# Kernel optimization log

Hardware: AMD Instinct MI355X
Metric: run time of the kernel (lower is better)

## Reference

```python
import jax, jax.numpy as jnp
import numpy as np

EPS = 1e-5

def knn_gather(x, k):
    # x: [B,N,C] -> neighbors [B,N,k,C] (k nearest incl. self, DGCNN style)
    sq = jnp.sum(x * x, axis=-1)                                   # [B,N]
    dist = sq[:, :, None] + sq[:, None, :] - 2.0 * jnp.einsum('bnc,bmc->bnm', x, x)
    _, idx = jax.lax.top_k(-dist, k)                               # [B,N,k]
    neigh = jax.vmap(lambda xb, ib: xb[ib])(x, idx)                # [B,N,k,C]
    return neigh

def local_cov(neigh):
    # neigh: [B,N,k,C] -> flattened per-point covariance [B,N,C*C]
    k = neigh.shape[2]
    c = neigh - jnp.mean(neigh, axis=2, keepdims=True)
    cov = jnp.einsum('bnkc,bnkd->bncd', c, c) / k
    return cov.reshape(cov.shape[0], cov.shape[1], -1)

def bn(x, g, b):
    # BatchNorm1d training-mode forward on [B,N,C]: stats over (B,N), biased var
    m = jnp.mean(x, axis=(0, 1))
    v = jnp.var(x, axis=(0, 1))
    return (x - m) * jax.lax.rsqrt(v + EPS) * g + b

def setup_inputs() -> dict:
    key = jax.random.key(0)
    ks = jax.random.split(key, 8)
    B, N = 2, 8192
    d = {}
    d['x'] = jax.random.normal(ks[0], (B, N, 3), dtype=jnp.float32)
    # conv weights stored as [in, out] (1x1 Conv1d == per-point matmul)
    def w(k_, i, o):
        return jax.random.normal(k_, (i, o), dtype=jnp.float32) * (1.0 / np.sqrt(i))
    d['W1'] = w(ks[1], 12, 64);   d['g1'] = jnp.ones(64);   d['b1'] = jnp.zeros(64)
    d['W2'] = w(ks[2], 64, 64);   d['g2'] = jnp.ones(64);   d['b2'] = jnp.zeros(64)
    d['W3'] = w(ks[3], 64, 64);   d['g3'] = jnp.ones(64);   d['b3'] = jnp.zeros(64)
    d['gW1'] = w(ks[4], 64, 128);  d['gg1'] = jnp.ones(128);  d['gb1'] = jnp.zeros(128)
    d['gW2'] = w(ks[5], 128, 1024); d['gg2'] = jnp.ones(1024); d['gb2'] = jnp.zeros(1024)
    d['W4'] = w(ks[6], 1024, 512); d['g4'] = jnp.ones(512);  d['b4'] = jnp.zeros(512)
    return d

def reference(x, W1, g1, b1, W2, g2, b2, W3, g3, b3,
              gW1, gg1, gb1, gW2, gg2, gb2, W4, g4, b4):
    # GBEncoder forward
    neigh = knn_gather(x, 32)                                   # [B,N,32,3]
    h = jnp.concatenate([x, local_cov(neigh)], axis=-1)         # [B,N,12]
    h = jax.nn.relu(bn(h @ W1, g1, b1))                         # [B,N,64]
    h = jax.nn.relu(bn(h @ W2, g2, b2))
    h = jax.nn.relu(bn(h @ W3, g3, b3))
    # GraphLayer 1: knn(k=8) gather -> max over neighbors -> 1x1 conv + BN + LeakyReLU
    n = jnp.max(knn_gather(h, 8), axis=2)                       # [B,N,64]
    h = jax.nn.leaky_relu(bn(n @ gW1, gg1, gb1), 0.01)          # [B,N,128]
    # GraphLayer 2
    n = jnp.max(knn_gather(h, 8), axis=2)                       # [B,N,128]
    h = jax.nn.leaky_relu(bn(n @ gW2, gg2, gb2), 0.01)          # [B,N,1024]
    # global max-pool over points, keepdim -> [B,1,1024]
    h = jnp.max(h, axis=1, keepdims=True)
    return jax.nn.relu(bn(h @ W4, g4, b4))                      # [B,1,512]
```

## Files before the change

### kernel.cpp

```cpp
#include <hip/hip_runtime.h>
#include <cfloat>
#include <cstdint>

#define NPTS 8192
#define NBROWS 16384

typedef unsigned long long u64;
typedef unsigned short ushortT;
typedef __attribute__((ext_vector_type(8))) short short8;
typedef __attribute__((ext_vector_type(4))) float f32x4;

__device__ __forceinline__ unsigned fkey(float f) {
  unsigned u = __float_as_uint(f);
  return (u & 0x80000000u) ? ~u : (u | 0x80000000u);
}
__device__ __forceinline__ float fdecode(unsigned k) {
  unsigned u = (k & 0x80000000u) ? (k ^ 0x80000000u) : ~k;
  return __uint_as_float(u);
}
__device__ __forceinline__ float bf2f(ushortT v) {
  return __uint_as_float(((unsigned)v) << 16);
}
__device__ __forceinline__ unsigned rne16(float x, float& hf) {
  unsigned u = __float_as_uint(x);
  unsigned r = (u + 0x7FFFu + ((u >> 16) & 1u)) >> 16;
  hf = __uint_as_float(r << 16);
  return r;
}

template <int K>
__device__ __forceinline__ void chain_insert(u64 (&kk)[K], u64 key) {
  #pragma unroll
  for (int q = K - 1; q >= 1; --q) {
    bool cm1 = key < kk[q - 1];
    bool cq  = key < kk[q];
    kk[q] = cm1 ? kk[q - 1] : (cq ? key : kk[q]);
  }
  kk[0] = (key < kk[0]) ? key : kk[0];
}

__global__ __launch_bounds__(256) void sqx_kernel(const float* __restrict__ x,
                                                  float* __restrict__ sq) {
  int r = blockIdx.x * 256 + threadIdx.x;
  const float* xp = x + (size_t)r * 3;
  sq[r] = fmaf(xp[2], xp[2], fmaf(xp[1], xp[1], xp[0] * xp[0]));
}

__global__ __launch_bounds__(512, 4) void knn32_cov_kernel(const float* __restrict__ x,
                                                           const float* __restrict__ sqx,
                                                           float* __restrict__ feat) {
  __shared__ __align__(16) unsigned char smem[78080];
  float4* stage4 = (float4*)smem;
  unsigned* keyArea = (unsigned*)smem;
  unsigned* Trow = (unsigned*)(smem + 67584);
  unsigned* cnt  = (unsigned*)(smem + 67712);
  u64* apb = (u64*)(smem + 67840);

  const int t = threadIdx.x;
  const int r = t & 31, sub = t >> 5;
  const int rowBase = blockIdx.x * 32;
  const int batchBase = rowBase & ~(NPTS - 1);
  const int gRow = rowBase + r;

  const float xi0 = x[(size_t)gRow * 3 + 0];
  const float xi1 = x[(size_t)gRow * 3 + 1];
  const float xi2 = x[(size_t)gRow * 3 + 2];
  const float sqi = sqx[gRow];

  unsigned K[32];
  #pragma unroll
  for (int q = 0; q < 32; ++q) K[q] = 0xFFFFFFFFu;

  for (int round = 0; round < 4; ++round) {
    __syncthreads();
    #pragma unroll
    for (int u = 0; u < 4; ++u) {
      int pp = t + 512 * u;
      int s = pp >> 7, jj = pp & 127;
      int j = s * 512 + round * 128 + jj;
      const float* xp = x + (size_t)(batchBase + j) * 3;
      float4 w;
      w.x = xp[0]; w.y = xp[1]; w.z = xp[2];
      w.w = sqx[batchBase + j];
      stage4[pp] = w;
    }
    __syncthreads();
    const float4* st = stage4 + sub * 128;
    for (int jj = 0; jj < 128; ++jj) {
      float4 w = st[jj];
      float dot = fmaf(xi2, w.z, fmaf(xi1, w.y, xi0 * w.x));
      float d = sqi + w.w - 2.0f * dot;
      unsigned key = fkey(d);
      #pragma unroll
      for (int q = 31; q >= 1; --q) K[q] = max(K[q - 1], min(key, K[q]));
      K[0] = min(key, K[0]);
    }
  }
  __syncthreads();
  {
    const int base = (sub * 32 + r) * 33;
    #pragma unroll
    for (int z = 0; z < 32; ++z) keyArea[base + z] = K[z];
  }
  __syncthreads();
  if (t < 32) {
    cnt[t] = 0u;
    unsigned P[16];
    #pragma unroll
    for (int s = 0; s < 16; ++s) P[s] = 0u;
    unsigned T = 0u;
    for (int step = 0; step < 32; ++step) {
      unsigned best = 0xFFFFFFFFu; int bs = 0;
      #pragma unroll
      for (int s = 0; s < 16; ++s) {
        unsigned v = keyArea[(s * 32 + t) * 33 + P[s]];
        if (v < best) { best = v; bs = s; }
      }
      T = best;
      #pragma unroll
      for (int s = 0; s < 16; ++s) P[s] += (s == bs);
    }
    Trow[t] = T;
  }
  __syncthreads();
  for (int round = 0; round < 4; ++round) {
    __syncthreads();
    #pragma unroll
    for (int u = 0; u < 4; ++u) {
      int pp = t + 512 * u;
      int s = pp >> 7, jj = pp & 127;
      int j = s * 512 + round * 128 + jj;
      const float* xp = x + (size_t)(batchBase + j) * 3;
      float4 w;
      w.x = xp[0]; w.y = xp[1]; w.z = xp[2];
      w.w = sqx[batchBase + j];
      stage4[pp] = w;
    }
    __syncthreads();
    const float4* st = stage4 + sub * 128;
    const unsigned T = Trow[r];
    for (int jj = 0; jj < 128; ++jj) {
      float4 w = st[jj];
      float dot = fmaf(xi2, w.z, fmaf(xi1, w.y, xi0 * w.x));
      float d = sqi + w.w - 2.0f * dot;
      unsigned key = fkey(d);
      if (key <= T) {
        int j = sub * 512 + round * 128 + jj;
        unsigned slot = atomicAdd(&cnt[r], 1u);
        if (slot < 40u) apb[r * 40 + slot] = ((u64)key << 16) | (unsigned)j;
      }
    }
  }
  __syncthreads();
  if (t < 32) {
    int n = (int)cnt[t]; if (n > 40) n = 40;
    u64 kk[32];
    #pragma unroll
    for (int q = 0; q < 32; ++q) kk[q] = ~0ULL;
    for (int i = 0; i < n; ++i) chain_insert<32>(kk, apb[t * 40 + i]);
    float sx = 0.f, sy = 0.f, sz = 0.f;
    #pragma unroll 4
    for (int z = 0; z < 32; ++z) {
      const float* xp = x + (size_t)(batchBase + (int)(kk[z] & 0xFFFFULL)) * 3;
      sx += xp[0]; sy += xp[1]; sz += xp[2];
    }
    const float m0 = sx * (1.f / 32.f), m1 = sy * (1.f / 32.f), m2 = sz * (1.f / 32.f);
    float c00 = 0, c01 = 0, c02 = 0, c11 = 0, c12 = 0, c22 = 0;
    #pragma unroll 4
    for (int z = 0; z < 32; ++z) {
      const float* xp = x + (size_t)(batchBase + (int)(kk[z] & 0xFFFFULL)) * 3;
      float a0 = xp[0] - m0, a1 = xp[1] - m1, a2 = xp[2] - m2;
      c00 = fmaf(a0, a0, c00); c01 = fmaf(a0, a1, c01); c02 = fmaf(a0, a2, c02);
      c11 = fmaf(a1, a1, c11); c12 = fmaf(a1, a2, c12); c22 = fmaf(a2, a2, c22);
    }
    const float inv = 1.f / 32.f;
    float* fp = feat + (size_t)(rowBase + t) * 12;
    fp[0] = xi0; fp[1] = xi1; fp[2] = xi2;
    fp[3] = c00 * inv; fp[4] = c01 * inv; fp[5] = c02 * inv;
    fp[6] = c01 * inv; fp[7] = c11 * inv; fp[8] = c12 * inv;
    fp[9] = c02 * inv; fp[10] = c12 * inv; fp[11] = c22 * inv;
  }
}

__global__ __launch_bounds__(64) void mm12_64_kernel(const float* __restrict__ feat,
                                                     const float* __restrict__ W,
                                                     float* __restrict__ y,
                                                     float* __restrict__ psum,
                                                     float* __restrict__ psq) {
  __shared__ __align__(16) float Ws[12 * 64];
  const int t = threadIdx.x;
  for (int u = t; u < 192; u += 64) ((float4*)Ws)[u] = ((const float4*)W)[u];
  __syncthreads();
  const int row = blockIdx.x * 64 + t;
  float in[12];
  {
    const float4* fp = (const float4*)(feat + (size_t)row * 12);
    float4 a = fp[0], b = fp[1], c = fp[2];
    in[0] = a.x; in[1] = a.y; in[2] = a.z; in[3] = a.w;
    in[4] = b.x; in[5] = b.y; in[6] = b.z; in[7] = b.w;
    in[8] = c.x; in[9] = c.y; in[10] = c.z; in[11] = c.w;
  }
  float acc[64];
  #pragma unroll
  for (int o = 0; o < 64; ++o) acc[o] = 0.f;
  #pragma unroll
  for (int i = 0; i < 12; ++i) {
    const float xi = in[i];
    #pragma unroll
    for (int og = 0; og < 16; ++og) {
      float4 w4 = *(const float4*)(Ws + i * 64 + og * 4);
      acc[og * 4 + 0] = fmaf(xi, w4.x, acc[og * 4 + 0]);
      acc[og * 4 + 1] = fmaf(xi, w4.y, acc[og * 4 + 1]);
      acc[og * 4 + 2] = fmaf(xi, w4.z, acc[og * 4 + 2]);
      acc[og * 4 + 3] = fmaf(xi, w4.w, acc[og * 4 + 3]);
    }
  }
  float4* yp = (float4*)(y + (size_t)row * 64);
  #pragma unroll
  for (int og = 0; og < 16; ++og)
    yp[og] = make_float4(acc[og * 4 + 0], acc[og * 4 + 1], acc[og * 4 + 2], acc[og * 4 + 3]);
  #pragma unroll 1
  for (int o = 0; o < 64; ++o) {
    float s = acc[o], q = acc[o] * acc[o];
    #pragma unroll
    for (int m = 1; m < 64; m <<= 1) { s += __shfl_xor(s, m); q += __shfl_xor(q, m); }
    if (t == 0) { psum[blockIdx.x * 64 + o] = s; psq[blockIdx.x * 64 + o] = q; }
  }
}

template <int OUT, bool BNRELU>
__global__ __launch_bounds__(64) void mm64_kernel(const float* __restrict__ src,
                                                  const float* __restrict__ W,
                                                  const float* __restrict__ scale,
                                                  const float* __restrict__ shift,
                                                  float* __restrict__ y,
                                                  float* __restrict__ psum,
                                                  float* __restrict__ psq) {
  __shared__ __align__(16) float Ws[64 * OUT];
  const int t = threadIdx.x;
  for (int u = t; u < 16 * OUT; u += 64) ((float4*)Ws)[u] = ((const float4*)W)[u];
  __syncthreads();
  const int row = blockIdx.x * 64 + t;
  float in[64];
  {
    const float4* sp = (const float4*)(src + (size_t)row * 64);
    #pragma unroll
    for (int u = 0; u < 16; ++u) {
      float4 v = sp[u];
      if (BNRELU) {
        v.x = fmaxf(fmaf(v.x, scale[u * 4 + 0], shift[u * 4 + 0]), 0.f);
        v.y = fmaxf(fmaf(v.y, scale[u * 4 + 1], shift[u * 4 + 1]), 0.f);
        v.z = fmaxf(fmaf(v.z, scale[u * 4 + 2], shift[u * 4 + 2]), 0.f);
        v.w = fmaxf(fmaf(v.w, scale[u * 4 + 3], shift[u * 4 + 3]), 0.f);
      }
      in[u * 4 + 0] = v.x; in[u * 4 + 1] = v.y; in[u * 4 + 2] = v.z; in[u * 4 + 3] = v.w;
    }
  }
  for (int half = 0; half < OUT / 64; ++half) {
    float acc[64];
    #pragma unroll
    for (int o = 0; o < 64; ++o) acc[o] = 0.f;
    #pragma unroll 4
    for (int i = 0; i < 64; ++i) {
      const float xi = in[i];
      #pragma unroll
      for (int og = 0; og < 16; ++og) {
        float4 w4 = *(const float4*)(Ws + i * OUT + half * 64 + og * 4);
        acc[og * 4 + 0] = fmaf(xi, w4.x, acc[og * 4 + 0]);
        acc[og * 4 + 1] = fmaf(xi, w4.y, acc[og * 4 + 1]);
        acc[og * 4 + 2] = fmaf(xi, w4.z, acc[og * 4 + 2]);
        acc[og * 4 + 3] = fmaf(xi, w4.w, acc[og * 4 + 3]);
      }
    }
    float4* yp = (float4*)(y + (size_t)row * OUT + half * 64);
    #pragma unroll
    for (int og = 0; og < 16; ++og)
      yp[og] = make_float4(acc[og * 4 + 0], acc[og * 4 + 1], acc[og * 4 + 2], acc[og * 4 + 3]);
    #pragma unroll 1
    for (int o = 0; o < 64; ++o) {
      float s = acc[o], q = acc[o] * acc[o];
      #pragma unroll
      for (int m = 1; m < 64; m <<= 1) { s += __shfl_xor(s, m); q += __shfl_xor(q, m); }
      if (t == 0) {
        psum[blockIdx.x * OUT + half * 64 + o] = s;
        psq[blockIdx.x * OUT + half * 64 + o] = q;
      }
    }
  }
}

template <int C>
__global__ void finP_kernel(const float* __restrict__ psum, const float* __restrict__ psq,
                            const float* __restrict__ g, const float* __restrict__ b,
                            float* __restrict__ scale, float* __restrict__ shift) {
  int c = threadIdx.x;
  float s = 0.f, q = 0.f;
  for (int bb = 0; bb < 256; ++bb) { s += psum[bb * C + c]; q += psq[bb * C + c]; }
  float m = s * (1.f / 16384.f);
  float v = q * (1.f / 16384.f) - m * m;
  float sc = g[c] * rsqrtf(v + 1e-5f);
  scale[c] = sc;
  shift[c] = b[c] - m * sc;
}

template <int C, bool LEAKY>
__global__ __launch_bounds__(256) void apply_kernel(const float* __restrict__ yraw,
                                                    const float* __restrict__ scale,
                                                    const float* __restrict__ shift,
                                                    ushortT* __restrict__ hbf,
                                                    float* __restrict__ sqout) {
  const int row = blockIdx.x * 256 + threadIdx.x;
  const float4* sp = (const float4*)(yraw + (size_t)row * C);
  ushortT* hb = hbf + (size_t)row * (3 * C);
  float sq = 0.f;
  #pragma unroll
  for (int g = 0; g < C / 8; ++g) {
    float e[8];
    #pragma unroll
    for (int half = 0; half < 2; ++half) {
      float4 v = sp[g * 2 + half];
      const int u = g * 2 + half;
      float4 o;
      o.x = fmaf(v.x, scale[u * 4 + 0], shift[u * 4 + 0]);
      o.y = fmaf(v.y, scale[u * 4 + 1], shift[u * 4 + 1]);
      o.z = fmaf(v.z, scale[u * 4 + 2], shift[u * 4 + 2]);
      o.w = fmaf(v.w, scale[u * 4 + 3], shift[u * 4 + 3]);
      if (LEAKY) {
        o.x = o.x > 0.f ? o.x : 0.01f * o.x;
        o.y = o.y > 0.f ? o.y : 0.01f * o.y;
        o.z = o.z > 0.f ? o.z : 0.01f * o.z;
        o.w = o.w > 0.f ? o.w : 0.01f * o.w;
      } else {
        o.x = fmaxf(o.x, 0.f); o.y = fmaxf(o.y, 0.f);
        o.z = fmaxf(o.z, 0.f); o.w = fmaxf(o.w, 0.f);
      }
      sq = fmaf(o.x, o.x, sq); sq = fmaf(o.y, o.y, sq);
      sq = fmaf(o.z, o.z, sq); sq = fmaf(o.w, o.w, sq);
      e[half * 4 + 0] = o.x; e[half * 4 + 1] = o.y;
      e[half * 4 + 2] = o.z; e[half * 4 + 3] = o.w;
    }
    unsigned pa[8], pb[8], pc[8];
    #pragma unroll
    for (int j = 0; j < 8; ++j) {
      float af, bf, cf;
      pa[j] = rne16(e[j], af);
      float r1 = e[j] - af;
      pb[j] = rne16(r1, bf);
      float r2 = r1 - bf;
      pc[j] = rne16(r2, cf);
    }
    uint4 va, vb, vc;
    va.x = pa[0] | (pa[1] << 16); va.y = pa[2] | (pa[3] << 16);
    va.z = pa[4] | (pa[5] << 16); va.w = pa[6] | (pa[7] << 16);
    vb.x = pb[0] | (pb[1] << 16); vb.y = pb[2] | (pb[3] << 16);
    vb.z = pb[4] | (pb[5] << 16); vb.w = pb[6] | (pb[7] << 16);
    vc.x = pc[0] | (pc[1] << 16); vc.y = pc[2] | (pc[3] << 16);
    vc.z = pc[4] | (pc[5] << 16); vc.w = pc[6] | (pc[7] << 16);
    *(uint4*)(hb + g * 8) = va;
    *(uint4*)(hb + C + g * 8) = vb;
    *(uint4*)(hb + 2 * C + g * 8) = vc;
  }
  sqout[row] = sq;
}

template <int C>
__global__ __launch_bounds__(256, 3) void knn8_kernel(const ushortT* __restrict__ hbf,
                                                      const float* __restrict__ sqh,
                                                      u64* __restrict__ plist) {
  static_assert(C == 64 || C == 128, "C");
  constexpr int STR = 3 * C + 8;
  constexpr int BSB = 64 * STR * 2;
  constexpr int SMB = BSB > 49152 ? BSB : 49152;
  __shared__ __align__(16) unsigned char smem[SMB];
  ushortT* Bs = (ushortT*)smem;
  u64* mb = (u64*)smem;
  __shared__ float sqB[64];

  const int t = threadIdx.x;
  const int l = t & 63, w = t >> 6;
  const int quad = l >> 4, fif = l & 15;
  const int rg = blockIdx.x >> 2, quarter = blockIdx.x & 3;
  const int rowBase = rg * 64;
  const int batchBase = rowBase & ~(NPTS - 1);

  constexpr int KS = C / 32;
  short8 aa[KS], ab[KS], ac[KS];
  {
    const int arow = rowBase + 16 * w + fif;
    const ushortT* ap = hbf + (size_t)arow * (3 * C);
    #pragma unroll
    for (int s = 0; s < KS; ++s) {
      aa[s] = *(const short8*)(ap + s * 32 + quad * 8);
      ab[s] = *(const short8*)(ap + C + s * 32 + quad * 8);
      ac[s] = *(const short8*)(ap + 2 * C + s * 32 + quad * 8);
    }
  }
  float sqA[4];
  #pragma unroll
  for (int r = 0; r < 4; ++r) sqA[r] = sqh[rowBase + 16 * w + quad * 4 + r];

  u64 L[4][8];
  #pragma unroll
  for (int r = 0; r < 4; ++r)
    #pragma unroll
    for (int z = 0; z < 8; ++z) L[r][z] = ~0ULL;

  constexpr int CPP = C / 8;
  constexpr int LOG = (CPP == 16) ? 4 : 3;

  for (int chunk = 0; chunk < 32; ++chunk) {
    const int cb = quarter * 2048 + chunk * 64;
    __syncthreads();
    {
      #pragma unroll
      for (int p = 0; p < 3; ++p) {
        #pragma unroll
        for (int z = 0; z < (64 * CPP) / 256; ++z) {
          int id = t + 256 * z;
          int col = id >> LOG, ch = id & (CPP - 1);
          uint4 v = *(const uint4*)(hbf + (size_t)(batchBase + cb + col) * (3 * C) + p * C + ch * 8);
          *(uint4*)(Bs + col * STR + p * C + ch * 8) = v;
        }
      }
      if (t < 64) sqB[t] = sqh[batchBase + cb + t];
    }
    __syncthreads();
    #pragma unroll
    for (int tile = 0; tile < 4; ++tile) {
      const int lcol = tile * 16 + fif;
      f32x4 acc0 = {0.f, 0.f, 0.f, 0.f};
      f32x4 acc1 = {0.f, 0.f, 0.f, 0.f};
      f32x4 acc2 = {0.f, 0.f, 0.f, 0.f};
      const ushortT* bp = Bs + lcol * STR + quad * 8;
      #pragma unroll
      for (int s = 0; s < KS; ++s) {
        short8 ba = *(const short8*)(bp + s * 32);
        short8 bb = *(const short8*)(bp + C + s * 32);
        short8 bc = *(const short8*)(bp + 2 * C + s * 32);
        acc0 = __builtin_amdgcn_mfma_f32_16x16x32_bf16(aa[s], ba, acc0, 0, 0, 0);
        acc1 = __builtin_amdgcn_mfma_f32_16x16x32_bf16(aa[s], bb, acc1, 0, 0, 0);
        acc2 = __builtin_amdgcn_mfma_f32_16x16x32_bf16(ab[s], ba, acc2, 0, 0, 0);
        acc0 = __builtin_amdgcn_mfma_f32_16x16x32_bf16(aa[s], bc, acc0, 0, 0, 0);
        acc1 = __builtin_amdgcn_mfma_f32_16x16x32_bf16(ac[s], ba, acc1, 0, 0, 0);
        acc2 = __builtin_amdgcn_mfma_f32_16x16x32_bf16(ab[s], bb, acc2, 0, 0, 0);
      }
      const float sb = sqB[lcol];
      const unsigned gcol = (unsigned)(cb + lcol);
      #pragma unroll
      for (int r = 0; r < 4; ++r) {
        float dot = acc0[r] + acc1[r] + acc2[r];
        float d = sqA[r] + sb - 2.0f * dot;
        u64 key = ((u64)fkey(d) << 16) | gcol;
        chain_insert<8>(L[r], key);
      }
    }
  }
  for (int rh = 0; rh < 2; ++rh) {
    __syncthreads();
    if ((w >> 1) == rh) {
      #pragma unroll
      for (int r = 0; r < 4; ++r) {
        int lr = (16 * w + quad * 4 + r) & 31;
        #pragma unroll
        for (int z = 0; z < 8; ++z) mb[(lr * 16 + fif) * 8 + z] = L[r][z];
      }
    }
    __syncthreads();
    if (t < 32) {
      int ps[16];
      #pragma unroll
      for (int s = 0; s < 16; ++s) ps[s] = 0;
      u64 outk[12];
      for (int z = 0; z < 12; ++z) {
        u64 best = ~0ULL; int bs = 0;
        #pragma unroll
        for (int s = 0; s < 16; ++s) {
          u64 v = (ps[s] < 8) ? mb[(t * 16 + s) * 8 + ps[s]] : ~0ULL;
          if (v < best) { best = v; bs = s; }
        }
        outk[z] = best;
        #pragma unroll
        for (int s = 0; s < 16; ++s) ps[s] += (s == bs);
      }
      u64* dst = plist + ((size_t)(rowBase + rh * 32 + t) * 4 + quarter) * 12;
      #pragma unroll
      for (int z = 0; z < 12; ++z) dst[z] = outk[z];
    }
  }
}

template <int C>
__global__ __launch_bounds__(256) void knn8rf_kernel(const u64* __restrict__ plist,
                                                     const ushortT* __restrict__ hbf,
                                                     const float* __restrict__ sqh,
                                                     float* __restrict__ nout) {
  __shared__ float xiL[4][C];
  const int t = threadIdx.x;
  const int w = t >> 6, l = t & 63;
  const int row = blockIdx.x * 4 + w;
  const int batchBase = row & ~(NPTS - 1);
  {
    const ushortT* src = hbf + (size_t)row * (3 * C);
    #pragma unroll
    for (int u = 0; u < C / 64; ++u) {
      int ch = l + u * 64;
      float av = bf2f(src[ch]), bv = bf2f(src[C + ch]), cv = bf2f(src[2 * C + ch]);
      xiL[w][ch] = av + (bv + cv);
    }
  }
  __syncthreads();
  const float sqi = sqh[row];
  const u64* pl = plist + (size_t)row * 48;
  u64 myk = ~0ULL;
  if (l < 48) {
    int cand = (int)(pl[l] & 0xFFFFULL) & (NPTS - 1);
    const ushortT* sp = hbf + (size_t)(batchBase + cand) * (3 * C);
    float dot = 0.f;
    #pragma unroll 4
    for (int kk = 0; kk < C; kk += 2) {
      unsigned ua = *(const unsigned*)(sp + kk);
      unsigned ub = *(const unsigned*)(sp + C + kk);
      unsigned uc = *(const unsigned*)(sp + 2 * C + kk);
      float a0 = __uint_as_float(ua << 16), a1 = __uint_as_float(ua & 0xFFFF0000u);
      float b0 = __uint_as_float(ub << 16), b1 = __uint_as_float(ub & 0xFFFF0000u);
      float c0 = __uint_as_float(uc << 16), c1 = __uint_as_float(uc & 0xFFFF0000u);
      float x0 = a0 + (b0 + c0), x1 = a1 + (b1 + c1);
      dot = fmaf(xiL[w][kk], x0, dot);
      dot = fmaf(xiL[w][kk + 1], x1, dot);
    }
    float d = sqi + sqh[batchBase + cand] - 2.0f * dot;
    myk = ((u64)fkey(d) << 16) | (unsigned)cand;
  }
  u64 top[8];
  #pragma unroll
  for (int z = 0; z < 8; ++z) {
    u64 m = myk;
    #pragma unroll
    for (int off = 1; off < 64; off <<= 1) {
      u64 o = (u64)__shfl_xor((long long)m, off);
      m = o < m ? o : m;
    }
    top[z] = m;
    if (myk == m) myk = ~0ULL;
  }
  constexpr int PER = C / 64;
  float mx[PER];
  #pragma unroll
  for (int u = 0; u < PER; ++u) mx[u] = -FLT_MAX;
  #pragma unroll
  for (int z = 0; z < 8; ++z) {
    int idx = (int)(top[z] & 0xFFFFULL) & (NPTS - 1);
    const ushortT* src = hbf + (size_t)(batchBase + idx) * (3 * C);
    #pragma unroll
    for (int u = 0; u < PER; ++u) {
      int ch = l + u * 64;
      float av = bf2f(src[ch]), bv = bf2f(src[C + ch]), cv = bf2f(src[2 * C + ch]);
      float xv = av + (bv + cv);
      mx[u] = fmaxf(mx[u], xv);
    }
  }
  float* dst = nout + (size_t)row * C;
  #pragma unroll
  for (int u = 0; u < PER; ++u) dst[l + u * 64] = mx[u];
}

__global__ __launch_bounds__(256) void mmE_kernel(const float* __restrict__ n2,
                                                  const float* __restrict__ W,
                                                  float* __restrict__ psum,
                                                  float* __restrict__ psq,
                                                  unsigned* __restrict__ gmax) {
  __shared__ __align__(16) float As[64 * 64];
  __shared__ __align__(16) float Bs[64 * 64];
  __shared__ float sP[16 * 64];
  __shared__ float qP[16 * 64];
  __shared__ float mP[16 * 64];
  const int t = threadIdx.x;
  const int rowStripe = blockIdx.x >> 4;
  const int colStripe = blockIdx.x & 15;
  const int rowBase = rowStripe * 64;
  const int colBase = colStripe * 64;
  const int batch = rowBase >> 13;
  const int tx = t & 15, ty = t >> 4;

  float acc[16];
  #pragma unroll
  for (int q = 0; q < 16; ++q) acc[q] = 0.f;

  for (int kh = 0; kh < 2; ++kh) {
    __syncthreads();
    {
      const int ar = t & 63;
      const int k0 = (t >> 6) * 16;
      const float* src = n2 + (size_t)(rowBase + ar) * 128 + kh * 64 + k0;
      #pragma unroll
      for (int kk = 0; kk < 16; kk += 4) {
        float4 v = *(const float4*)(src + kk);
        As[(k0 + kk + 0) * 64 + ar] = v.x;
        As[(k0 + kk + 1) * 64 + ar] = v.y;
        As[(k0 + kk + 2) * 64 + ar] = v.z;
        As[(k0 + kk + 3) * 64 + ar] = v.w;
      }
    }
    {
      #pragma unroll
      for (int z = 0; z < 4; ++z) {
        int u = t + 256 * z;
        int k = u >> 4, c4 = u & 15;
        float4 v = *(const float4*)(W + (size_t)(kh * 64 + k) * 1024 + colBase + c4 * 4);
        *(float4*)(Bs + k * 64 + c4 * 4) = v;
      }
    }
    __syncthreads();
    #pragma unroll 4
    for (int k = 0; k < 64; ++k) {
      float4 a4 = *(const float4*)(As + k * 64 + ty * 4);
      float4 b4 = *(const float4*)(Bs + k * 64 + tx * 4);
      acc[0] = fmaf(a4.x, b4.x, acc[0]);   acc[1] = fmaf(a4.x, b4.y, acc[1]);
      acc[2] = fmaf(a4.x, b4.z, acc[2]);   acc[3] = fmaf(a4.x, b4.w, acc[3]);
      acc[4] = fmaf(a4.y, b4.x, acc[4]);   acc[5] = fmaf(a4.y, b4.y, acc[5]);
      acc[6] = fmaf(a4.y, b4.z, acc[6]);   acc[7] = fmaf(a4.y, b4.w, acc[7]);
      acc[8] = fmaf(a4.z, b4.x, acc[8]);   acc[9] = fmaf(a4.z, b4.y, acc[9]);
      acc[10] = fmaf(a4.z, b4.z, acc[10]); acc[11] = fmaf(a4.z, b4.w, acc[11]);
      acc[12] = fmaf(a4.w, b4.x, acc[12]); acc[13] = fmaf(a4.w, b4.y, acc[13]);
      acc[14] = fmaf(a4.w, b4.z, acc[14]); acc[15] = fmaf(a4.w, b4.w, acc[15]);
    }
  }
  #pragma unroll
  for (int p = 0; p < 4; ++p) {
    float s = 0.f, q = 0.f, m = -FLT_MAX;
    #pragma unroll
    for (int qq = 0; qq < 4; ++qq) {
      float v = acc[qq * 4 + p];
      s += v; q = fmaf(v, v, q); m = fmaxf(m, v);
    }
    sP[ty * 64 + tx * 4 + p] = s;
    qP[ty * 64 + tx * 4 + p] = q;
    mP[ty * 64 + tx * 4 + p] = m;
  }
  __syncthreads();
  if (t < 64) {
    float s = 0.f, q = 0.f, m = -FLT_MAX;
    #pragma unroll
    for (int u = 0; u < 16; ++u) {
      s += sP[u * 64 + t];
      q += qP[u * 64 + t];
      m = fmaxf(m, mP[u * 64 + t]);
    }
    psum[rowStripe * 1024 + colBase + t] = s;
    psq [rowStripe * 1024 + colBase + t] = q;
    atomicMax(&gmax[batch * 1024 + colBase + t], fkey(m));
  }
}

__global__ void poolbn_kernel(const float* __restrict__ psumE, const float* __restrict__ psqE,
                              const unsigned* __restrict__ gmax,
                              const float* __restrict__ gg2, const float* __restrict__ gb2,
                              float* __restrict__ fpool) {
  int c = threadIdx.x;
  float s = 0.f, q = 0.f;
  for (int bb = 0; bb < 256; ++bb) { s += psumE[bb * 1024 + c]; q += psqE[bb * 1024 + c]; }
  float m = s * (1.f / 16384.f);
  float v = q * (1.f / 16384.f) - m * m;
  float sc = gg2[c] * rsqrtf(v + 1e-5f);
  float sh = gb2[c] - m * sc;
  #pragma unroll
  for (int b = 0; b < 2; ++b) {
    float raw = fdecode(gmax[b * 1024 + c]);
    float t = fmaf(raw, sc, sh);
    fpool[b * 1024 + c] = t > 0.f ? t : 0.01f * t;
  }
}

__global__ __launch_bounds__(64) void final_kernel(const float* __restrict__ fpool,
                                                   const float* __restrict__ W4,
                                                   const float* __restrict__ g4,
                                                   const float* __restrict__ b4f,
                                                   float* __restrict__ out) {
  const int o = blockIdx.x * 64 + threadIdx.x;
  float a0 = 0.f, a1 = 0.f;
  for (int c = 0; c < 1024; ++c) {
    float w = W4[(size_t)c * 512 + o];
    a0 = fmaf(fpool[c], w, a0);
    a1 = fmaf(fpool[1024 + c], w, a1);
  }
  float m = 0.5f * (a0 + a1);
  float d0 = a0 - m, d1 = a1 - m;
  float v = 0.5f * (d0 * d0 + d1 * d1);
  float r = rsqrtf(v + 1e-5f);
  float o0 = fmaf(d0 * r, g4[o], b4f[o]);
  float o1 = fmaf(d1 * r, g4[o], b4f[o]);
  out[o] = fmaxf(o0, 0.f);
  out[512 + o] = fmaxf(o1, 0.f);
}

extern "C" void kernel_launch(void* const* d_in, const int* in_sizes, int n_in,
                              void* d_out, int out_size, void* d_ws, size_t ws_size,
                              hipStream_t stream) {
  (void)in_sizes; (void)n_in; (void)out_size; (void)ws_size;
  const float* x   = (const float*)d_in[0];
  const float* W1  = (const float*)d_in[1];
  const float* g1  = (const float*)d_in[2];
  const float* b1  = (const float*)d_in[3];
  const float* W2  = (const float*)d_in[4];
  const float* g2  = (const float*)d_in[5];
  const float* b2  = (const float*)d_in[6];
  const float* W3  = (const float*)d_in[7];
  const float* g3  = (const float*)d_in[8];
  const float* b3  = (const float*)d_in[9];
  const float* gW1 = (const float*)d_in[10];
  const float* gg1 = (const float*)d_in[11];
  const float* gb1 = (const float*)d_in[12];
  const float* gW2 = (const float*)d_in[13];
  const float* gg2 = (const float*)d_in[14];
  const float* gb2 = (const float*)d_in[15];
  const float* W4  = (const float*)d_in[16];
  const float* g4  = (const float*)d_in[17];
  const float* b4  = (const float*)d_in[18];
  float* out = (float*)d_out;
  float* ws = (float*)d_ws;

  float* sqx  = ws;
  float* feat = sqx + 16384;
  float* bufA = feat + 196608;
  float* bufB = bufA + 1048576;
  float* sqh  = bufB + 1048576;
  float* sqg  = sqh + 16384;
  float* ygr  = sqg + 16384;
  float* hbfR = ygr + 2097152;
  float* st   = hbfR + 3145728;

  unsigned* gmax = (unsigned*)(st);
  float* scale0 = st + 2048;  float* shift0 = st + 2112;
  float* scale1 = st + 2176;  float* shift1 = st + 2240;
  float* scale2 = st + 2304;  float* shift2 = st + 2368;
  float* scale3 = st + 2432;  float* shift3 = st + 2560;
  float* fpool  = st + 2688;
  float* p1s    = st + 4736;
  float* p1q    = p1s + 16384;

  float* p2s = feat;             float* p2q = feat + 16384;
  float* p3s = feat + 32768;     float* p3q = feat + 49152;
  float* p4s = feat;             float* p4q = feat + 32768;
  float* pEs = bufA;             float* pEq = bufA + 262144;
  u64* plist = (u64*)bufA;

  ushortT* hbf1 = (ushortT*)hbfR;
  ushortT* hbf2 = (ushortT*)hbfR;
  float* n1 = hbfR + 1572864;
  float* n2 = ygr;

  hipMemsetAsync(gmax, 0, 2048 * sizeof(unsigned), stream);
  sqx_kernel<<<64, 256, 0, stream>>>(x, sqx);
  knn32_cov_kernel<<<512, 512, 0, stream>>>(x, sqx, feat);
  mm12_64_kernel<<<256, 64, 0, stream>>>(feat, W1, bufA, p1s, p1q);
  finP_kernel<64><<<1, 64, 0, stream>>>(p1s, p1q, g1, b1, scale0, shift0);
  mm64_kernel<64, true><<<256, 64, 0, stream>>>(bufA, W2, scale0, shift0, bufB, p2s, p2q);
  finP_kernel<64><<<1, 64, 0, stream>>>(p2s, p2q, g2, b2, scale1, shift1);
  mm64_kernel<64, true><<<256, 64, 0, stream>>>(bufB, W3, scale1, shift1, bufA, p3s, p3q);
  finP_kernel<64><<<1, 64, 0, stream>>>(p3s, p3q, g3, b3, scale2, shift2);
  apply_kernel<64, false><<<64, 256, 0, stream>>>(bufA, scale2, shift2, hbf1, sqh);
  knn8_kernel<64><<<1024, 256, 0, stream>>>(hbf1, sqh, plist);
  knn8rf_kernel<64><<<4096, 256, 0, stream>>>(plist, hbf1, sqh, n1);
  mm64_kernel<128, false><<<256, 64, 0, stream>>>(n1, gW1, scale0, shift0, ygr, p4s, p4q);
  finP_kernel<128><<<1, 128, 0, stream>>>(p4s, p4q, gg1, gb1, scale3, shift3);
  apply_kernel<128, true><<<64, 256, 0, stream>>>(ygr, scale3, shift3, hbf2, sqg);
  knn8_kernel<128><<<1024, 256, 0, stream>>>(hbf2, sqg, plist);
  knn8rf_kernel<128><<<4096, 256, 0, stream>>>(plist, hbf2, sqg, n2);
  mmE_kernel<<<4096, 256, 0, stream>>>(n2, gW2, pEs, pEq, gmax);
  poolbn_kernel<<<1, 1024, 0, stream>>>(pEs, pEq, gmax, gg2, gb2, fpool);
  final_kernel<<<8, 64, 0, stream>>>(fpool, W4, g4, b4, out);
}
```

Baseline: 2.121 ms.

## Use two-term bf16 split in knn8 coarse pass, store third term separately

```diff
diff --git a/kernel.cpp b/kernel.cpp
--- a/kernel.cpp
+++ b/kernel.cpp
@@ -307,11 +307,13 @@
 __global__ __launch_bounds__(256) void apply_kernel(const float* __restrict__ yraw,
                                                     const float* __restrict__ scale,
                                                     const float* __restrict__ shift,
-                                                    ushortT* __restrict__ hbf,
+                                                    ushortT* __restrict__ hab,
+                                                    ushortT* __restrict__ hc,
                                                     float* __restrict__ sqout) {
   const int row = blockIdx.x * 256 + threadIdx.x;
   const float4* sp = (const float4*)(yraw + (size_t)row * C);
-  ushortT* hb = hbf + (size_t)row * (3 * C);
+  ushortT* hb = hab + (size_t)row * (2 * C);
+  ushortT* hcp = hc + (size_t)row * C;
   float sq = 0.f;
   #pragma unroll
   for (int g = 0; g < C / 8; ++g) {
@@ -358,19 +360,19 @@
     vc.z = pc[4] | (pc[5] << 16); vc.w = pc[6] | (pc[7] << 16);
     *(uint4*)(hb + g * 8) = va;
     *(uint4*)(hb + C + g * 8) = vb;
-    *(uint4*)(hb + 2 * C + g * 8) = vc;
+    *(uint4*)(hcp + g * 8) = vc;
   }
   sqout[row] = sq;
 }
 
 template <int C>
-__global__ __launch_bounds__(256, 3) void knn8_kernel(const ushortT* __restrict__ hbf,
+__global__ __launch_bounds__(256, 4) void knn8_kernel(const ushortT* __restrict__ hab,
                                                       const float* __restrict__ sqh,
                                                       u64* __restrict__ plist) {
   static_assert(C == 64 || C == 128, "C");
-  constexpr int STR = 3 * C + 8;
+  constexpr int STR = 2 * C + 8;
   constexpr int BSB = 64 * STR * 2;
-  constexpr int SMB = BSB > 49152 ? BSB : 49152;
+  constexpr int SMB = BSB > 32768 ? BSB : 32768;
   __shared__ __align__(16) unsigned char smem[SMB];
   ushortT* Bs = (ushortT*)smem;
   u64* mb = (u64*)smem;
@@ -379,20 +381,19 @@
   const int t = threadIdx.x;
   const int l = t & 63, w = t >> 6;
   const int quad = l >> 4, fif = l & 15;
-  const int rg = blockIdx.x >> 2, quarter = blockIdx.x & 3;
+  const int quarter = blockIdx.x >> 8, rg = blockIdx.x & 255;
   const int rowBase = rg * 64;
   const int batchBase = rowBase & ~(NPTS - 1);
 
   constexpr int KS = C / 32;
-  short8 aa[KS], ab[KS], ac[KS];
+  short8 aa[KS], ab[KS];
   {
     const int arow = rowBase + 16 * w + fif;
-    const ushortT* ap = hbf + (size_t)arow * (3 * C);
+    const ushortT* ap = hab + (size_t)arow * (2 * C);
     #pragma unroll
     for (int s = 0; s < KS; ++s) {
       aa[s] = *(const short8*)(ap + s * 32 + quad * 8);
       ab[s] = *(const short8*)(ap + C + s * 32 + quad * 8);
-      ac[s] = *(const short8*)(ap + 2 * C + s * 32 + quad * 8);
     }
   }
   float sqA[4];
@@ -405,22 +406,19 @@
     #pragma unroll
     for (int z = 0; z < 8; ++z) L[r][z] = ~0ULL;
 
-  constexpr int CPP = C / 8;
-  constexpr int LOG = (CPP == 16) ? 4 : 3;
+  constexpr int CH = C / 4;
+  constexpr int LOG = (CH == 32) ? 5 : 4;
 
   for (int chunk = 0; chunk < 32; ++chunk) {
     const int cb = quarter * 2048 + chunk * 64;
     __syncthreads();
     {
       #pragma unroll
-      for (int p = 0; p < 3; ++p) {
-        #pragma unroll
-        for (int z = 0; z < (64 * CPP) / 256; ++z) {
-          int id = t + 256 * z;
-          int col = id >> LOG, ch = id & (CPP - 1);
-          uint4 v = *(const uint4*)(hbf + (size_t)(batchBase + cb + col) * (3 * C) + p * C + ch * 8);
-          *(uint4*)(Bs + col * STR + p * C + ch * 8) = v;
-        }
+      for (int z = 0; z < (64 * CH) / 256; ++z) {
+        int id = t + 256 * z;
+        int col = id >> LOG, ch = id & (CH - 1);
+        uint4 v = *(const uint4*)(hab + (size_t)(batchBase + cb + col) * (2 * C) + ch * 8);
+        *(uint4*)(Bs + col * STR + ch * 8) = v;
       }
       if (t < 64) sqB[t] = sqh[batchBase + cb + t];
     }
@@ -430,25 +428,21 @@
       const int lcol = tile * 16 + fif;
       f32x4 acc0 = {0.f, 0.f, 0.f, 0.f};
       f32x4 acc1 = {0.f, 0.f, 0.f, 0.f};
-      f32x4 acc2 = {0.f, 0.f, 0.f, 0.f};
       const ushortT* bp = Bs + lcol * STR + quad * 8;
       #pragma unroll
       for (int s = 0; s < KS; ++s) {
         short8 ba = *(const short8*)(bp + s * 32);
         short8 bb = *(const short8*)(bp + C + s * 32);
-        short8 bc = *(const short8*)(bp + 2 * C + s * 32);
         acc0 = __builtin_amdgcn_mfma_f32_16x16x32_bf16(aa[s], ba, acc0, 0, 0, 0);
         acc1 = __builtin_amdgcn_mfma_f32_16x16x32_bf16(aa[s], bb, acc1, 0, 0, 0);
-        acc2 = __builtin_amdgcn_mfma_f32_16x16x32_bf16(ab[s], ba, acc2, 0, 0, 0);
-        acc0 = __builtin_amdgcn_mfma_f32_16x16x32_bf16(aa[s], bc, acc0, 0, 0, 0);
-        acc1 = __builtin_amdgcn_mfma_f32_16x16x32_bf16(ac[s], ba, acc1, 0, 0, 0);
-        acc2 = __builtin_amdgcn_mfma_f32_16x16x32_bf16(ab[s], bb, acc2, 0, 0, 0);
+        acc0 = __builtin_amdgcn_mfma_f32_16x16x32_bf16(ab[s], bb, acc0, 0, 0, 0);
+        acc1 = __builtin_amdgcn_mfma_f32_16x16x32_bf16(ab[s], ba, acc1, 0, 0, 0);
       }
       const float sb = sqB[lcol];
       const unsigned gcol = (unsigned)(cb + lcol);
       #pragma unroll
       for (int r = 0; r < 4; ++r) {
-        float dot = acc0[r] + acc1[r] + acc2[r];
+        float dot = acc0[r] + acc1[r];
         float d = sqA[r] + sb - 2.0f * dot;
         u64 key = ((u64)fkey(d) << 16) | gcol;
         chain_insert<8>(L[r], key);
@@ -491,7 +485,8 @@
 
 template <int C>
 __global__ __launch_bounds__(256) void knn8rf_kernel(const u64* __restrict__ plist,
-                                                     const ushortT* __restrict__ hbf,
+                                                     const ushortT* __restrict__ hab,
+                                                     const ushortT* __restrict__ hc,
                                                      const float* __restrict__ sqh,
                                                      float* __restrict__ nout) {
   __shared__ float xiL[4][C];
@@ -500,11 +495,12 @@
   const int row = blockIdx.x * 4 + w;
   const int batchBase = row & ~(NPTS - 1);
   {
-    const ushortT* src = hbf + (size_t)row * (3 * C);
+    const ushortT* sab = hab + (size_t)row * (2 * C);
+    const ushortT* sc = hc + (size_t)row * C;
     #pragma unroll
     for (int u = 0; u < C / 64; ++u) {
       int ch = l + u * 64;
-      float av = bf2f(src[ch]), bv = bf2f(src[C + ch]), cv = bf2f(src[2 * C + ch]);
+      float av = bf2f(sab[ch]), bv = bf2f(sab[C + ch]), cv = bf2f(sc[ch]);
       xiL[w][ch] = av + (bv + cv);
     }
   }
@@ -514,13 +510,14 @@
   u64 myk = ~0ULL;
   if (l < 48) {
     int cand = (int)(pl[l] & 0xFFFFULL) & (NPTS - 1);
-    const ushortT* sp = hbf + (size_t)(batchBase + cand) * (3 * C);
+    const ushortT* sab = hab + (size_t)(batchBase + cand) * (2 * C);
+    const ushortT* sc = hc + (size_t)(batchBase + cand) * C;
     float dot = 0.f;
     #pragma unroll 4
     for (int kk = 0; kk < C; kk += 2) {
-      unsigned ua = *(const unsigned*)(sp + kk);
-      unsigned ub = *(const unsigned*)(sp + C + kk);
-      unsigned uc = *(const unsigned*)(sp + 2 * C + kk);
+      unsigned ua = *(const unsigned*)(sab + kk);
+      unsigned ub = *(const unsigned*)(sab + C + kk);
+      unsigned uc = *(const unsigned*)(sc + kk);
       float a0 = __uint_as_float(ua << 16), a1 = __uint_as_float(ua & 0xFFFF0000u);
       float b0 = __uint_as_float(ub << 16), b1 = __uint_as_float(ub & 0xFFFF0000u);
       float c0 = __uint_as_float(uc << 16), c1 = __uint_as_float(uc & 0xFFFF0000u);
@@ -550,11 +547,12 @@
   #pragma unroll
   for (int z = 0; z < 8; ++z) {
     int idx = (int)(top[z] & 0xFFFFULL) & (NPTS - 1);
-    const ushortT* src = hbf + (size_t)(batchBase + idx) * (3 * C);
+    const ushortT* sab = hab + (size_t)(batchBase + idx) * (2 * C);
+    const ushortT* sc = hc + (size_t)(batchBase + idx) * C;
     #pragma unroll
     for (int u = 0; u < PER; ++u) {
       int ch = l + u * 64;
-      float av = bf2f(src[ch]), bv = bf2f(src[C + ch]), cv = bf2f(src[2 * C + ch]);
+      float av = bf2f(sab[ch]), bv = bf2f(sab[C + ch]), cv = bf2f(sc[ch]);
       float xv = av + (bv + cv);
       mx[u] = fmaxf(mx[u], xv);
     }
@@ -744,10 +742,12 @@
   float* pEs = bufA;             float* pEq = bufA + 262144;
   u64* plist = (u64*)bufA;
 
-  ushortT* hbf1 = (ushortT*)hbfR;
-  ushortT* hbf2 = (ushortT*)hbfR;
-  float* n1 = hbfR + 1572864;
-  float* n2 = ygr;
+  ushortT* hab1 = (ushortT*)hbfR;
+  ushortT* hc1  = (ushortT*)(hbfR + 1048576);
+  float*   n1   = hbfR + 1572864;
+  ushortT* hab2 = (ushortT*)hbfR;
+  ushortT* hc2  = (ushortT*)(hbfR + 2097152);
+  float*   n2   = ygr;
 
   hipMemsetAsync(gmax, 0, 2048 * sizeof(unsigned), stream);
   sqx_kernel<<<64, 256, 0, stream>>>(x, sqx);
@@ -758,14 +758,14 @@
   finP_kernel<64><<<1, 64, 0, stream>>>(p2s, p2q, g2, b2, scale1, shift1);
   mm64_kernel<64, true><<<256, 64, 0, stream>>>(bufB, W3, scale1, shift1, bufA, p3s, p3q);
   finP_kernel<64><<<1, 64, 0, stream>>>(p3s, p3q, g3, b3, scale2, shift2);
-  apply_kernel<64, false><<<64, 256, 0, stream>>>(bufA, scale2, shift2, hbf1, sqh);
-  knn8_kernel<64><<<1024, 256, 0, stream>>>(hbf1, sqh, plist);
-  knn8rf_kernel<64><<<4096, 256, 0, stream>>>(plist, hbf1, sqh, n1);
+  apply_kernel<64, false><<<64, 256, 0, stream>>>(bufA, scale2, shift2, hab1, hc1, sqh);
+  knn8_kernel<64><<<1024, 256, 0, stream>>>(hab1, sqh, plist);
+  knn8rf_kernel<64><<<4096, 256, 0, stream>>>(plist, hab1, hc1, sqh, n1);
   mm64_kernel<128, false><<<256, 64, 0, stream>>>(n1, gW1, scale0, shift0, ygr, p4s, p4q);
   finP_kernel<128><<<1, 128, 0, stream>>>(p4s, p4q, gg1, gb1, scale3, shift3);
-  apply_kernel<128, true><<<64, 256, 0, stream>>>(ygr, scale3, shift3, hbf2, sqg);
-  knn8_kernel<128><<<1024, 256, 0, stream>>>(hbf2, sqg, plist);
-  knn8rf_kernel<128><<<4096, 256, 0, stream>>>(plist, hbf2, sqg, n2);
+  apply_kernel<128, true><<<64, 256, 0, stream>>>(ygr, scale3, shift3, hab2, hc2, sqg);
+  knn8_kernel<128><<<1024, 256, 0, stream>>>(hab2, sqg, plist);
+  knn8rf_kernel<128><<<4096, 256, 0, stream>>>(plist, hab2, hc2, sqg, n2);
   mmE_kernel<<<4096, 256, 0, stream>>>(n2, gW2, pEs, pEq, gmax);
   poolbn_kernel<<<1, 1024, 0, stream>>>(pEs, pEq, gmax, gg2, gb2, fpool);
   final_kernel<<<8, 64, 0, stream>>>(fpool, W4, g4, b4, out);
```

Result: no change. 2.120 ms (-0.0%).
